# Performance work log

Hardware: AMD Instinct MI355X
Metric: run time of the kernel (lower is better)

## Reference

```python
import jax, jax.numpy as jnp
import numpy as np
from jax import lax

EPS = 1e-8


def _moving_average(x, window):
    # x: [B, T]; replicate-pad left by window-1, then mean-filter (matches F.pad(mode='replicate') + conv1d)
    pad = jnp.repeat(x[:, :1], window - 1, axis=1)
    xp = jnp.concatenate([pad, x], axis=1)[:, None, :]          # [B, 1, T+w-1]
    k = (jnp.ones((1, 1, window), x.dtype) / window)
    out = lax.conv_general_dilated(xp, k, (1,), 'VALID')         # [B, 1, T]
    return out[:, 0, :]


def _ema(x, period):
    # linear recurrence ema[t] = a*x[t] + (1-a)*ema[t-1], ema[0] = x[0]
    alpha = 2.0 / (period + 1)
    def step(carry, xt):
        y = alpha * xt + (1.0 - alpha) * carry
        return y, y
    init = x[:, 0]
    _, ys = lax.scan(step, init, x[:, 1:].T)                     # ys: [T-1, B]
    return jnp.concatenate([x[:, :1], ys.T], axis=1)


def _rsi(close, period=14):
    delta = jnp.diff(close, axis=1, prepend=close[:, :1])
    gain = jnp.where(delta > 0, delta, 0.0)
    loss = jnp.where(delta < 0, -delta, 0.0)
    avg_gain = _moving_average(gain, period)
    avg_loss = _moving_average(loss, period)
    rs = avg_gain / (avg_loss + EPS)
    return 100.0 - 100.0 / (1.0 + rs)


def _macd(close, fast=12, slow=26, signal=9):
    ema_fast = _ema(close, fast)
    ema_slow = _ema(close, slow)
    macd = ema_fast - ema_slow
    signal_line = _ema(macd, signal)
    return macd, signal_line


def _bollinger(close, period=20, num_std=2.0):
    ma = _moving_average(close, period)
    mean = _moving_average(close, period)
    sq_diff = (close - mean) ** 2
    variance = _moving_average(sq_diff, period)
    std = jnp.sqrt(variance + EPS)
    return ma + num_std * std, ma, ma - num_std * std


def _atr(close, period=14):
    high_low = jnp.abs(jnp.diff(close, axis=1, prepend=close[:, :1]))
    return _moving_average(high_low, period)


def _forward(close, volume):
    outs = []
    for window in (5, 10, 20, 50):
        ma = _moving_average(close, window)
        outs.append(ma)
        outs.append(close / (ma + EPS))
    outs.append(_rsi(close, 14))
    macd, signal = _macd(close)
    outs.append(macd)
    outs.append(signal)
    outs.append(macd - signal)
    bb_u, bb_m, bb_l = _bollinger(close, 20)
    outs.append(bb_u)
    outs.append(bb_m)
    outs.append(bb_l)
    outs.append((close - bb_l) / (bb_u - bb_l + EPS))
    outs.append(_atr(close, 14))
    return jnp.stack(outs)                                        # [17, B, T]


def setup_inputs() -> dict:
    key = jax.random.key(0)
    k1, k2 = jax.random.split(key)
    B, T = 512, 8192
    close = jax.random.uniform(k1, (B, T), dtype=jnp.float32)
    volume = jax.random.uniform(k2, (B, T), dtype=jnp.float32)
    return {"close": close, "volume": volume}


def reference(close, volume):
    return _forward(close, volume)
```

## Files before the change

kernel.cpp:

```cpp
#include <hip/hip_runtime.h>
#include <cstddef>

#define NTHREADS 256
#define TROW 8192
#define NROWS 512
#define TILE 1024
#define HALO 256
#define REG 1280
#define CHUNK 5
#define KOUT 4
#define FEPS 1e-8f

static_assert(REG == TILE + HALO, "region");
static_assert(CHUNK * NTHREADS == REG, "chunk");
static_assert(KOUT * NTHREADS == TILE, "kout");

__device__ __forceinline__ float pow_chunk(float b) {
  float b2 = b * b;
  return b2 * b2 * b;
}

template <typename SRC>
__device__ __forceinline__ void block_prefix(SRC src, float* __restrict__ dst,
                                             int tid, int lane, int wid,
                                             float* __restrict__ sc) {
  const int c0 = tid * CHUNK;
  float tot = 0.f;
#pragma unroll
  for (int k = 0; k < CHUNK; ++k) tot += src(c0 + k);
  float x = tot;
#pragma unroll
  for (int off = 1; off < 64; off <<= 1) {
    float y = __shfl_up(x, off, 64);
    if (lane >= off) x += y;
  }
  if (lane == 63) sc[wid] = x;
  __syncthreads();
  float woff = 0.f;
  for (int w = 0; w < wid; ++w) woff += sc[w];
  float run = woff + x - tot;
  if (tid == 0) dst[0] = 0.f;
#pragma unroll
  for (int k = 0; k < CHUNK; ++k) { run += src(c0 + k); dst[c0 + k + 1] = run; }
  __syncthreads();
}

__global__ __launch_bounds__(NTHREADS) void feat_kernel(
    const float* __restrict__ close, float* __restrict__ out) {
  __shared__ float cl[REG];
  __shared__ float Qa[REG + 1];
  __shared__ float Qb[REG + 1];
  __shared__ float sc[16];

  const int tid = threadIdx.x;
  const int lane = tid & 63;
  const int wid = tid >> 6;
  const int j = blockIdx.x;
  const int r = blockIdx.y;
  const int out_start = j * TILE;
  const int s = (j == 0) ? 0 : (out_start - HALO);
  const int ob = out_start - s;
  const size_t BT = (size_t)NROWS * TROW;
  const size_t rbase = (size_t)r * TROW + (size_t)s;

  const float* rp = close + rbase;
#pragma unroll
  for (int k = 0; k < CHUNK; ++k) {
    int i = tid + k * NTHREADS;
    cl[i] = rp[i];
  }
  __syncthreads();
  const float c0v = cl[0];

  block_prefix([&](int i) { return cl[i]; }, Qa, tid, lane, wid, sc);

#pragma unroll
  for (int k = 0; k < KOUT; ++k) {
    const int i = ob + tid + k * NTHREADS;
    const size_t base = rbase + (size_t)i;
    const float c = cl[i];
    const float q1 = Qa[i + 1];
#pragma unroll
    for (int wi = 0; wi < 4; ++wi) {
      const int w = (wi == 0) ? 5 : (wi == 1) ? 10 : (wi == 2) ? 20 : 50;
      const float invw = 1.f / (float)w;
      int al = i + 1 - w;
      float pad = 0.f;
      if (al < 0) { pad = (float)(-al) * c0v; al = 0; }
      const float ma = (q1 - Qa[al] + pad) * invw;
      out[(size_t)(2 * wi) * BT + base] = ma;
      out[(size_t)(2 * wi + 1) * BT + base] = c / (ma + FEPS);
    }
  }

  const bool first = (j == 0);
  block_prefix(
      [&](int i) -> float {
        if (!first && i < 19) return 0.f;
        int al = i - 19;
        float pad = 0.f;
        if (al < 0) { pad = (float)(-al) * c0v; al = 0; }
        const float m = (Qa[i + 1] - Qa[al] + pad) * 0.05f;
        const float d = cl[i] - m;
        return d * d;
      },
      Qb, tid, lane, wid, sc);

#pragma unroll
  for (int k = 0; k < KOUT; ++k) {
    const int i = ob + tid + k * NTHREADS;
    const size_t base = rbase + (size_t)i;
    const float c = cl[i];
    int al = i - 19;
    float pad = 0.f;
    if (al < 0) { pad = (float)(-al) * c0v; al = 0; }
    const float ma20 = (Qa[i + 1] - Qa[al] + pad) * 0.05f;
    int av = i - 19;
    if (av < 0) av = 0;
    float vs = Qb[i + 1] - Qb[av];
    vs = fmaxf(vs, 0.f);
    const float sd = sqrtf(vs * 0.05f + FEPS);
    const float up = ma20 + 2.f * sd;
    const float lo = ma20 - 2.f * sd;
    out[12 * BT + base] = up;
    out[13 * BT + base] = ma20;
    out[14 * BT + base] = lo;
    out[15 * BT + base] = (c - lo) / (up - lo + FEPS);
  }
  __syncthreads();

  block_prefix(
      [&](int i) -> float { return (i == 0) ? 0.f : fabsf(cl[i] - cl[i - 1]); },
      Qa, tid, lane, wid, sc);

#pragma unroll
  for (int k = 0; k < KOUT; ++k) {
    const int i = ob + tid + k * NTHREADS;
    const size_t base = rbase + (size_t)i;
    const float c = cl[i];
    int ar = i - 13;
    if (ar < 0) ar = 0;
    int ap = ar - 1;
    if (ap < 0) ap = 0;
    const float sabs = Qa[i + 1] - Qa[ar];
    const float sdel = c - cl[ap];
    const float g = (sabs + sdel) * (0.5f / 14.f);
    const float l = (sabs - sdel) * (0.5f / 14.f);
    const float rs = g / (l + FEPS);
    out[8 * BT + base] = 100.f - 100.f / (1.f + rs);
    out[16 * BT + base] = sabs * (1.f / 14.f);
  }

  {
    const float a12 = 2.f / 13.f, b12 = 11.f / 13.f;
    const float a26 = 2.f / 27.f, b26 = 25.f / 27.f;
    const int c0 = tid * CHUNK;
    float y1 = 0.f, y2 = 0.f;
#pragma unroll
    for (int k = 0; k < CHUNK; ++k) {
      const float x = cl[c0 + k];
      if (c0 + k == 0) { y1 = x; y2 = x; }
      else {
        y1 = fmaf(b12, y1, a12 * x);
        y2 = fmaf(b26, y2, a26 * x);
      }
    }
    float A1 = (tid == 0) ? 0.f : pow_chunk(b12);
    float A2 = (tid == 0) ? 0.f : pow_chunk(b26);
    float B1 = y1, B2 = y2;
#pragma unroll
    for (int off = 1; off < 64; off <<= 1) {
      const float pA1 = __shfl_up(A1, off, 64), pB1 = __shfl_up(B1, off, 64);
      const float pA2 = __shfl_up(A2, off, 64), pB2 = __shfl_up(B2, off, 64);
      if (lane >= off) {
        B1 = fmaf(A1, pB1, B1); A1 *= pA1;
        B2 = fmaf(A2, pB2, B2); A2 *= pA2;
      }
    }
    float eA1 = __shfl_up(A1, 1, 64), eB1 = __shfl_up(B1, 1, 64);
    float eA2 = __shfl_up(A2, 1, 64), eB2 = __shfl_up(B2, 1, 64);
    if (lane == 0) { eA1 = 1.f; eB1 = 0.f; eA2 = 1.f; eB2 = 0.f; }
    if (lane == 63) {
      sc[wid * 4 + 0] = A1; sc[wid * 4 + 1] = B1;
      sc[wid * 4 + 2] = A2; sc[wid * 4 + 3] = B2;
    }
    __syncthreads();
    float cB1 = 0.f, cB2 = 0.f;
    for (int w = 0; w < wid; ++w) {
      cB1 = fmaf(sc[w * 4 + 0], cB1, sc[w * 4 + 1]);
      cB2 = fmaf(sc[w * 4 + 2], cB2, sc[w * 4 + 3]);
    }
    y1 = fmaf(eA1, cB1, eB1);
    y2 = fmaf(eA2, cB2, eB2);
#pragma unroll
    for (int k = 0; k < CHUNK; ++k) {
      const float x = cl[c0 + k];
      if (c0 + k == 0) { y1 = x; y2 = x; }
      else {
        y1 = fmaf(b12, y1, a12 * x);
        y2 = fmaf(b26, y2, a26 * x);
      }
      Qb[c0 + k] = y1 - y2;
    }
    __syncthreads();
  }

  {
    const float a9 = 0.2f, b9 = 0.8f;
    const int c0 = tid * CHUNK;
    float y = 0.f;
#pragma unroll
    for (int k = 0; k < CHUNK; ++k) {
      const float x = Qb[c0 + k];
      if (c0 + k == 0) y = x;
      else y = fmaf(b9, y, a9 * x);
    }
    float A = (tid == 0) ? 0.f : pow_chunk(b9);
    float Bv = y;
#pragma unroll
    for (int off = 1; off < 64; off <<= 1) {
      const float pA = __shfl_up(A, off, 64), pB = __shfl_up(Bv, off, 64);
      if (lane >= off) { Bv = fmaf(A, pB, Bv); A *= pA; }
    }
    float eA = __shfl_up(A, 1, 64), eB = __shfl_up(Bv, 1, 64);
    if (lane == 0) { eA = 1.f; eB = 0.f; }
    if (lane == 63) { sc[wid * 2] = A; sc[wid * 2 + 1] = Bv; }
    __syncthreads();
    float cB = 0.f;
    for (int w = 0; w < wid; ++w) cB = fmaf(sc[w * 2], cB, sc[w * 2 + 1]);
    y = fmaf(eA, cB, eB);
#pragma unroll
    for (int k = 0; k < CHUNK; ++k) {
      const float x = Qb[c0 + k];
      if (c0 + k == 0) y = x;
      else y = fmaf(b9, y, a9 * x);
      Qa[c0 + k] = y;
    }
    __syncthreads();
  }

#pragma unroll
  for (int k = 0; k < KOUT; ++k) {
    const int i = ob + tid + k * NTHREADS;
    const size_t base = rbase + (size_t)i;
    const float m = Qb[i];
    const float sg = Qa[i];
    out[9 * BT + base] = m;
    out[10 * BT + base] = sg;
    out[11 * BT + base] = m - sg;
  }
}

extern "C" void kernel_launch(void* const* d_in, const int* in_sizes, int n_in,
                              void* d_out, int out_size, void* d_ws, size_t ws_size,
                              hipStream_t stream) {
  (void)in_sizes; (void)n_in; (void)out_size; (void)d_ws; (void)ws_size;
  const float* close = (const float*)d_in[0];
  float* out = (float*)d_out;
  dim3 grid(TROW / TILE, NROWS, 1);
  feat_kernel<<<grid, dim3(NTHREADS, 1, 1), 0, stream>>>(close, out);
}
```

Before: 302.3 us.

## Buffer all feature outputs in registers and emit vectorized nontemporal stores

Each thread now owns four contiguous time steps instead of four strided ones. It keeps all 17 feature values in a register array and writes them at the end as 128-bit nontemporal stores, one per feature plane. The input tile load is also vectorized to float4, and one redundant __syncthreads between the Bollinger and ATR stages is dropped. The aim is fewer, wider store instructions and less cache pollution from the large write-only output. The cost is higher register pressure from holding 68 floats per thread, which could reduce occupancy.

```diff
diff --git a/kernel.cpp b/kernel.cpp
--- a/kernel.cpp
+++ b/kernel.cpp
@@ -8,12 +8,14 @@
 #define HALO 256
 #define REG 1280
 #define CHUNK 5
-#define KOUT 4
+#define VE 4
 #define FEPS 1e-8f
 
 static_assert(REG == TILE + HALO, "region");
 static_assert(CHUNK * NTHREADS == REG, "chunk");
-static_assert(KOUT * NTHREADS == TILE, "kout");
+static_assert(VE * NTHREADS == TILE, "ve");
+
+typedef float f32x4 __attribute__((ext_vector_type(4)));
 
 __device__ __forceinline__ float pow_chunk(float b) {
   float b2 = b * b;
@@ -47,7 +49,7 @@
 
 __global__ __launch_bounds__(NTHREADS) void feat_kernel(
     const float* __restrict__ close, float* __restrict__ out) {
-  __shared__ float cl[REG];
+  __shared__ __align__(16) float cl[REG];
   __shared__ float Qa[REG + 1];
   __shared__ float Qb[REG + 1];
   __shared__ float sc[16];
@@ -63,21 +65,23 @@
   const size_t BT = (size_t)NROWS * TROW;
   const size_t rbase = (size_t)r * TROW + (size_t)s;
 
-  const float* rp = close + rbase;
-#pragma unroll
-  for (int k = 0; k < CHUNK; ++k) {
-    int i = tid + k * NTHREADS;
-    cl[i] = rp[i];
+  {
+    const f32x4* rp4 = reinterpret_cast<const f32x4*>(close + rbase);
+    f32x4* cl4 = reinterpret_cast<f32x4*>(cl);
+    cl4[tid] = rp4[tid];
+    if (tid < (REG / 4 - NTHREADS)) cl4[NTHREADS + tid] = rp4[NTHREADS + tid];
   }
   __syncthreads();
   const float c0v = cl[0];
 
+  float st[17][VE];
+  const int i0 = ob + VE * tid;
+
   block_prefix([&](int i) { return cl[i]; }, Qa, tid, lane, wid, sc);
 
 #pragma unroll
-  for (int k = 0; k < KOUT; ++k) {
-    const int i = ob + tid + k * NTHREADS;
-    const size_t base = rbase + (size_t)i;
+  for (int k = 0; k < VE; ++k) {
+    const int i = i0 + k;
     const float c = cl[i];
     const float q1 = Qa[i + 1];
 #pragma unroll
@@ -88,8 +92,8 @@
       float pad = 0.f;
       if (al < 0) { pad = (float)(-al) * c0v; al = 0; }
       const float ma = (q1 - Qa[al] + pad) * invw;
-      out[(size_t)(2 * wi) * BT + base] = ma;
-      out[(size_t)(2 * wi + 1) * BT + base] = c / (ma + FEPS);
+      st[2 * wi][k] = ma;
+      st[2 * wi + 1][k] = c / (ma + FEPS);
     }
   }
 
@@ -107,9 +111,8 @@
       Qb, tid, lane, wid, sc);
 
 #pragma unroll
-  for (int k = 0; k < KOUT; ++k) {
-    const int i = ob + tid + k * NTHREADS;
-    const size_t base = rbase + (size_t)i;
+  for (int k = 0; k < VE; ++k) {
+    const int i = i0 + k;
     const float c = cl[i];
     int al = i - 19;
     float pad = 0.f;
@@ -122,21 +125,19 @@
     const float sd = sqrtf(vs * 0.05f + FEPS);
     const float up = ma20 + 2.f * sd;
     const float lo = ma20 - 2.f * sd;
-    out[12 * BT + base] = up;
-    out[13 * BT + base] = ma20;
-    out[14 * BT + base] = lo;
-    out[15 * BT + base] = (c - lo) / (up - lo + FEPS);
-  }
-  __syncthreads();
+    st[12][k] = up;
+    st[13][k] = ma20;
+    st[14][k] = lo;
+    st[15][k] = (c - lo) / (up - lo + FEPS);
+  }
 
   block_prefix(
       [&](int i) -> float { return (i == 0) ? 0.f : fabsf(cl[i] - cl[i - 1]); },
       Qa, tid, lane, wid, sc);
 
 #pragma unroll
-  for (int k = 0; k < KOUT; ++k) {
-    const int i = ob + tid + k * NTHREADS;
-    const size_t base = rbase + (size_t)i;
+  for (int k = 0; k < VE; ++k) {
+    const int i = i0 + k;
     const float c = cl[i];
     int ar = i - 13;
     if (ar < 0) ar = 0;
@@ -147,8 +148,8 @@
     const float g = (sabs + sdel) * (0.5f / 14.f);
     const float l = (sabs - sdel) * (0.5f / 14.f);
     const float rs = g / (l + FEPS);
-    out[8 * BT + base] = 100.f - 100.f / (1.f + rs);
-    out[16 * BT + base] = sabs * (1.f / 14.f);
+    st[8][k] = 100.f - 100.f / (1.f + rs);
+    st[16][k] = sabs * (1.f / 14.f);
   }
 
   {
@@ -240,14 +241,22 @@
   }
 
 #pragma unroll
-  for (int k = 0; k < KOUT; ++k) {
-    const int i = ob + tid + k * NTHREADS;
-    const size_t base = rbase + (size_t)i;
+  for (int k = 0; k < VE; ++k) {
+    const int i = i0 + k;
     const float m = Qb[i];
     const float sg = Qa[i];
-    out[9 * BT + base] = m;
-    out[10 * BT + base] = sg;
-    out[11 * BT + base] = m - sg;
+    st[9][k] = m;
+    st[10][k] = sg;
+    st[11][k] = m - sg;
+  }
+
+  {
+    float* op = out + rbase + (size_t)i0;
+#pragma unroll
+    for (int f = 0; f < 17; ++f) {
+      f32x4 v = { st[f][0], st[f][1], st[f][2], st[f][3] };
+      __builtin_nontemporal_store(v, reinterpret_cast<f32x4*>(op + (size_t)f * BT));
+    }
   }
 }
 
```

Result: slower. 314.1 us (+3.9%).

## Fuse block prefix scans and EMA scans into two combined passes

Applied to the files above, without the earlier changes.

Merges the five separate block-wide scans (close prefix sum, abs-delta prefix sum, EMA12/26, variance prefix, EMA9) into two combined scan phases that share shuffles and barriers, keeping per-thread chunk values in registers. It also vectorises the global load of the close tile with float4. The aim is fewer __syncthreads and LDS round trips in a kernel that is largely bound by output writes. The cost is more shared memory (extra M and Sg arrays) and higher register pressure, which could lower occupancy.

```diff
diff --git a/kernel.cpp b/kernel.cpp
--- a/kernel.cpp
+++ b/kernel.cpp
@@ -15,42 +15,21 @@
 static_assert(CHUNK * NTHREADS == REG, "chunk");
 static_assert(KOUT * NTHREADS == TILE, "kout");
 
+typedef float f32x4 __attribute__((ext_vector_type(4)));
+
 __device__ __forceinline__ float pow_chunk(float b) {
   float b2 = b * b;
   return b2 * b2 * b;
 }
 
-template <typename SRC>
-__device__ __forceinline__ void block_prefix(SRC src, float* __restrict__ dst,
-                                             int tid, int lane, int wid,
-                                             float* __restrict__ sc) {
-  const int c0 = tid * CHUNK;
-  float tot = 0.f;
-#pragma unroll
-  for (int k = 0; k < CHUNK; ++k) tot += src(c0 + k);
-  float x = tot;
-#pragma unroll
-  for (int off = 1; off < 64; off <<= 1) {
-    float y = __shfl_up(x, off, 64);
-    if (lane >= off) x += y;
-  }
-  if (lane == 63) sc[wid] = x;
-  __syncthreads();
-  float woff = 0.f;
-  for (int w = 0; w < wid; ++w) woff += sc[w];
-  float run = woff + x - tot;
-  if (tid == 0) dst[0] = 0.f;
-#pragma unroll
-  for (int k = 0; k < CHUNK; ++k) { run += src(c0 + k); dst[c0 + k + 1] = run; }
-  __syncthreads();
-}
-
 __global__ __launch_bounds__(NTHREADS) void feat_kernel(
     const float* __restrict__ close, float* __restrict__ out) {
-  __shared__ float cl[REG];
+  __shared__ __align__(16) float cl[REG];
   __shared__ float Qa[REG + 1];
-  __shared__ float Qb[REG + 1];
-  __shared__ float sc[16];
+  __shared__ float Qd[REG + 1];
+  __shared__ float M[REG];
+  __shared__ float Sg[REG];
+  __shared__ float sc[24];
 
   const int tid = threadIdx.x;
   const int lane = tid & 63;
@@ -63,16 +42,92 @@
   const size_t BT = (size_t)NROWS * TROW;
   const size_t rbase = (size_t)r * TROW + (size_t)s;
 
-  const float* rp = close + rbase;
-#pragma unroll
-  for (int k = 0; k < CHUNK; ++k) {
-    int i = tid + k * NTHREADS;
-    cl[i] = rp[i];
+  {
+    const f32x4* rp4 = reinterpret_cast<const f32x4*>(close + rbase);
+    f32x4* cl4 = reinterpret_cast<f32x4*>(cl);
+    cl4[tid] = rp4[tid];
+    if (tid < (REG / 4 - NTHREADS)) cl4[NTHREADS + tid] = rp4[NTHREADS + tid];
   }
   __syncthreads();
   const float c0v = cl[0];
-
-  block_prefix([&](int i) { return cl[i]; }, Qa, tid, lane, wid, sc);
+  const int c0 = tid * CHUNK;
+
+  const float a12 = 2.f / 13.f, b12 = 11.f / 13.f;
+  const float a26 = 2.f / 27.f, b26 = 25.f / 27.f;
+  const float a9 = 0.2f, b9 = 0.8f;
+
+  float xk[CHUNK];
+  float dk[CHUNK];
+  float mreg[CHUNK];
+
+  {
+    const float xm1 = (c0 == 0) ? 0.f : cl[c0 - 1];
+    float prev = xm1;
+    float s_c = 0.f, s_a = 0.f, y1 = 0.f, y2 = 0.f;
+#pragma unroll
+    for (int k = 0; k < CHUNK; ++k) {
+      const int i = c0 + k;
+      const float x = cl[i];
+      xk[k] = x;
+      const float d = (i == 0) ? 0.f : fabsf(x - prev);
+      dk[k] = d;
+      prev = x;
+      s_c += x;
+      s_a += d;
+      if (i == 0) { y1 = x; y2 = x; }
+      else { y1 = fmaf(b12, y1, a12 * x); y2 = fmaf(b26, y2, a26 * x); }
+    }
+    float xc = s_c, xa = s_a;
+    float A1 = (tid == 0) ? 0.f : pow_chunk(b12);
+    float A2 = (tid == 0) ? 0.f : pow_chunk(b26);
+    float B1 = y1, B2 = y2;
+#pragma unroll
+    for (int off = 1; off < 64; off <<= 1) {
+      const float pc = __shfl_up(xc, off, 64);
+      const float pa = __shfl_up(xa, off, 64);
+      const float pA1 = __shfl_up(A1, off, 64), pB1 = __shfl_up(B1, off, 64);
+      const float pA2 = __shfl_up(A2, off, 64), pB2 = __shfl_up(B2, off, 64);
+      if (lane >= off) {
+        xc += pc; xa += pa;
+        B1 = fmaf(A1, pB1, B1); A1 *= pA1;
+        B2 = fmaf(A2, pB2, B2); A2 *= pA2;
+      }
+    }
+    float eA1 = __shfl_up(A1, 1, 64), eB1 = __shfl_up(B1, 1, 64);
+    float eA2 = __shfl_up(A2, 1, 64), eB2 = __shfl_up(B2, 1, 64);
+    if (lane == 0) { eA1 = 1.f; eB1 = 0.f; eA2 = 1.f; eB2 = 0.f; }
+    if (lane == 63) {
+      sc[wid * 6 + 0] = xc; sc[wid * 6 + 1] = xa;
+      sc[wid * 6 + 2] = A1; sc[wid * 6 + 3] = B1;
+      sc[wid * 6 + 4] = A2; sc[wid * 6 + 5] = B2;
+    }
+    __syncthreads();
+    float woc = 0.f, woa = 0.f, cB1 = 0.f, cB2 = 0.f;
+    for (int w = 0; w < wid; ++w) {
+      woc += sc[w * 6 + 0];
+      woa += sc[w * 6 + 1];
+      cB1 = fmaf(sc[w * 6 + 2], cB1, sc[w * 6 + 3]);
+      cB2 = fmaf(sc[w * 6 + 4], cB2, sc[w * 6 + 5]);
+    }
+    float rc = woc + xc - s_c;
+    float ra = woa + xa - s_a;
+    y1 = fmaf(eA1, cB1, eB1);
+    y2 = fmaf(eA2, cB2, eB2);
+    if (tid == 0) { Qa[0] = 0.f; Qd[0] = 0.f; }
+#pragma unroll
+    for (int k = 0; k < CHUNK; ++k) {
+      const int i = c0 + k;
+      const float x = xk[k];
+      rc += x;     Qa[i + 1] = rc;
+      ra += dk[k]; Qd[i + 1] = ra;
+      if (i == 0) { y1 = x; y2 = x; }
+      else { y1 = fmaf(b12, y1, a12 * x); y2 = fmaf(b26, y2, a26 * x); }
+      const float mm = y1 - y2;
+      M[i] = mm;
+      mreg[k] = mm;
+    }
+    __syncthreads();
+  }
 
 #pragma unroll
   for (int k = 0; k < KOUT; ++k) {
@@ -91,20 +146,75 @@
       out[(size_t)(2 * wi) * BT + base] = ma;
       out[(size_t)(2 * wi + 1) * BT + base] = c / (ma + FEPS);
     }
+    int ar = i - 13;
+    if (ar < 0) ar = 0;
+    int ap = ar - 1;
+    if (ap < 0) ap = 0;
+    const float sabs = Qd[i + 1] - Qd[ar];
+    const float sdel = c - cl[ap];
+    const float g = (sabs + sdel) * (0.5f / 14.f);
+    const float l = (sabs - sdel) * (0.5f / 14.f);
+    const float rs = g / (l + FEPS);
+    out[8 * BT + base] = 100.f - 100.f / (1.f + rs);
+    out[16 * BT + base] = sabs * (1.f / 14.f);
+    out[9 * BT + base] = M[i];
   }
 
   const bool first = (j == 0);
-  block_prefix(
-      [&](int i) -> float {
-        if (!first && i < 19) return 0.f;
+  {
+    float vq[CHUNK];
+    float s_q = 0.f, y9 = 0.f;
+#pragma unroll
+    for (int k = 0; k < CHUNK; ++k) {
+      const int i = c0 + k;
+      float v = 0.f;
+      if (first || i >= 19) {
         int al = i - 19;
         float pad = 0.f;
         if (al < 0) { pad = (float)(-al) * c0v; al = 0; }
-        const float m = (Qa[i + 1] - Qa[al] + pad) * 0.05f;
-        const float d = cl[i] - m;
-        return d * d;
-      },
-      Qb, tid, lane, wid, sc);
+        const float m20 = (Qa[i + 1] - Qa[al] + pad) * 0.05f;
+        const float dd = xk[k] - m20;
+        v = dd * dd;
+      }
+      vq[k] = v;
+      s_q += v;
+      const float xm = mreg[k];
+      if (i == 0) y9 = xm;
+      else y9 = fmaf(b9, y9, a9 * xm);
+    }
+    float xq = s_q;
+    float A = (tid == 0) ? 0.f : pow_chunk(b9);
+    float Bv = y9;
+#pragma unroll
+    for (int off = 1; off < 64; off <<= 1) {
+      const float pq = __shfl_up(xq, off, 64);
+      const float pA = __shfl_up(A, off, 64), pB = __shfl_up(Bv, off, 64);
+      if (lane >= off) { xq += pq; Bv = fmaf(A, pB, Bv); A *= pA; }
+    }
+    float eA = __shfl_up(A, 1, 64), eB = __shfl_up(Bv, 1, 64);
+    if (lane == 0) { eA = 1.f; eB = 0.f; }
+    if (lane == 63) { sc[wid * 3 + 0] = xq; sc[wid * 3 + 1] = A; sc[wid * 3 + 2] = Bv; }
+    __syncthreads();
+    float woq = 0.f, cB = 0.f;
+    for (int w = 0; w < wid; ++w) {
+      woq += sc[w * 3 + 0];
+      cB = fmaf(sc[w * 3 + 1], cB, sc[w * 3 + 2]);
+    }
+    float rq = woq + xq - s_q;
+    y9 = fmaf(eA, cB, eB);
+    if (tid == 0) Qd[0] = 0.f;
+#pragma unroll
+    for (int k = 0; k < CHUNK; ++k) {
+      const int i = c0 + k;
+      rq += vq[k];
+      Qd[i + 1] = rq;
+      const float xm = mreg[k];
+      if (i == 0) y9 = xm;
+      else y9 = fmaf(b9, y9, a9 * xm);
+      Sg[i] = y9;
+    }
+    __syncthreads();
+  }
 
 #pragma unroll
   for (int k = 0; k < KOUT; ++k) {
@@ -117,7 +227,7 @@
     const float ma20 = (Qa[i + 1] - Qa[al] + pad) * 0.05f;
     int av = i - 19;
     if (av < 0) av = 0;
-    float vs = Qb[i + 1] - Qb[av];
+    float vs = Qd[i + 1] - Qd[av];
     vs = fmaxf(vs, 0.f);
     const float sd = sqrtf(vs * 0.05f + FEPS);
     const float up = ma20 + 2.f * sd;
@@ -126,126 +236,8 @@
     out[13 * BT + base] = ma20;
     out[14 * BT + base] = lo;
     out[15 * BT + base] = (c - lo) / (up - lo + FEPS);
-  }
-  __syncthreads();
-
-  block_prefix(
-      [&](int i) -> float { return (i == 0) ? 0.f : fabsf(cl[i] - cl[i - 1]); },
-      Qa, tid, lane, wid, sc);
-
-#pragma unroll
-  for (int k = 0; k < KOUT; ++k) {
-    const int i = ob + tid + k * NTHREADS;
-    const size_t base = rbase + (size_t)i;
-    const float c = cl[i];
-    int ar = i - 13;
-    if (ar < 0) ar = 0;
-    int ap = ar - 1;
-    if (ap < 0) ap = 0;
-    const float sabs = Qa[i + 1] - Qa[ar];
-    const float sdel = c - cl[ap];
-    const float g = (sabs + sdel) * (0.5f / 14.f);
-    const float l = (sabs - sdel) * (0.5f / 14.f);
-    const float rs = g / (l + FEPS);
-    out[8 * BT + base] = 100.f - 100.f / (1.f + rs);
-    out[16 * BT + base] = sabs * (1.f / 14.f);
-  }
-
-  {
-    const float a12 = 2.f / 13.f, b12 = 11.f / 13.f;
-    const float a26 = 2.f / 27.f, b26 = 25.f / 27.f;
-    const int c0 = tid * CHUNK;
-    float y1 = 0.f, y2 = 0.f;
-#pragma unroll
-    for (int k = 0; k < CHUNK; ++k) {
-      const float x = cl[c0 + k];
-      if (c0 + k == 0) { y1 = x; y2 = x; }
-      else {
-        y1 = fmaf(b12, y1, a12 * x);
-        y2 = fmaf(b26, y2, a26 * x);
-      }
-    }
-    float A1 = (tid == 0) ? 0.f : pow_chunk(b12);
-    float A2 = (tid == 0) ? 0.f : pow_chunk(b26);
-    float B1 = y1, B2 = y2;
-#pragma unroll
-    for (int off = 1; off < 64; off <<= 1) {
-      const float pA1 = __shfl_up(A1, off, 64), pB1 = __shfl_up(B1, off, 64);
-      const float pA2 = __shfl_up(A2, off, 64), pB2 = __shfl_up(B2, off, 64);
-      if (lane >= off) {
-        B1 = fmaf(A1, pB1, B1); A1 *= pA1;
-        B2 = fmaf(A2, pB2, B2); A2 *= pA2;
-      }
-    }
-    float eA1 = __shfl_up(A1, 1, 64), eB1 = __shfl_up(B1, 1, 64);
-    float eA2 = __shfl_up(A2, 1, 64), eB2 = __shfl_up(B2, 1, 64);
-    if (lane == 0) { eA1 = 1.f; eB1 = 0.f; eA2 = 1.f; eB2 = 0.f; }
-    if (lane == 63) {
-      sc[wid * 4 + 0] = A1; sc[wid * 4 + 1] = B1;
-      sc[wid * 4 + 2] = A2; sc[wid * 4 + 3] = B2;
-    }
-    __syncthreads();
-    float cB1 = 0.f, cB2 = 0.f;
-    for (int w = 0; w < wid; ++w) {
-      cB1 = fmaf(sc[w * 4 + 0], cB1, sc[w * 4 + 1]);
-      cB2 = fmaf(sc[w * 4 + 2], cB2, sc[w * 4 + 3]);
-    }
-    y1 = fmaf(eA1, cB1, eB1);
-    y2 = fmaf(eA2, cB2, eB2);
-#pragma unroll
-    for (int k = 0; k < CHUNK; ++k) {
-      const float x = cl[c0 + k];
-      if (c0 + k == 0) { y1 = x; y2 = x; }
-      else {
-        y1 = fmaf(b12, y1, a12 * x);
-        y2 = fmaf(b26, y2, a26 * x);
-      }
-      Qb[c0 + k] = y1 - y2;
-    }
-    __syncthreads();
-  }
-
-  {
-    const float a9 = 0.2f, b9 = 0.8f;
-    const int c0 = tid * CHUNK;
-    float y = 0.f;
-#pragma unroll
-    for (int k = 0; k < CHUNK; ++k) {
-      const float x = Qb[c0 + k];
-      if (c0 + k == 0) y = x;
-      else y = fmaf(b9, y, a9 * x);
-    }
-    float A = (tid == 0) ? 0.f : pow_chunk(b9);
-    float Bv = y;
-#pragma unroll
-    for (int off = 1; off < 64; off <<= 1) {
-      const float pA = __shfl_up(A, off, 64), pB = __shfl_up(Bv, off, 64);
-      if (lane >= off) { Bv = fmaf(A, pB, Bv); A *= pA; }
-    }
-    float eA = __shfl_up(A, 1, 64), eB = __shfl_up(Bv, 1, 64);
-    if (lane == 0) { eA = 1.f; eB = 0.f; }
-    if (lane == 63) { sc[wid * 2] = A; sc[wid * 2 + 1] = Bv; }
-    __syncthreads();
-    float cB = 0.f;
-    for (int w = 0; w < wid; ++w) cB = fmaf(sc[w * 2], cB, sc[w * 2 + 1]);
-    y = fmaf(eA, cB, eB);
-#pragma unroll
-    for (int k = 0; k < CHUNK; ++k) {
-      const float x = Qb[c0 + k];
-      if (c0 + k == 0) y = x;
-      else y = fmaf(b9, y, a9 * x);
-      Qa[c0 + k] = y;
-    }
-    __syncthreads();
-  }
-
-#pragma unroll
-  for (int k = 0; k < KOUT; ++k) {
-    const int i = ob + tid + k * NTHREADS;
-    const size_t base = rbase + (size_t)i;
-    const float m = Qb[i];
-    const float sg = Qa[i];
-    out[9 * BT + base] = m;
+    const float sg = Sg[i];
+    const float m = M[i];
     out[10 * BT + base] = sg;
     out[11 * BT + base] = m - sg;
   }
```

Result: no change. 303.0 us (+0.2%).
